# Performance work log

Measured on AMD Instinct MI355X. Metric: run time of the kernel, lower is better.

## Reference

```python
import jax, jax.numpy as jnp
import numpy as np
from jax.scipy.special import logsumexp

B, T, S, V = 64, 1024, 512, 1024


def setup_inputs() -> dict:
    key = jax.random.key(0)
    k_obs, k_emis, k_trans, k_prior = jax.random.split(key, 4)
    observations = jax.random.randint(k_obs, (B, T), 0, V, dtype=jnp.int32)
    emission_table = jax.random.normal(k_emis, (V, S), dtype=jnp.float32)
    transitions = jax.random.normal(k_trans, (S, S), dtype=jnp.float32)
    prior = jax.random.normal(k_prior, (S,), dtype=jnp.float32)
    return {
        "observations": observations,
        "emission_table": emission_table,
        "transitions": transitions,
        "prior": prior,
    }


def reference(observations, emission_table, transitions, prior):
    # alpha_0[b, s] = emission_logits(obs_0)[b, s] + prior[s]
    alpha0 = emission_table[observations[:, 0]] + prior  # [B, S]

    def step(alpha, obs_t):
        # new_alpha[b, j] = emis[b, j] + logsumexp_i(alpha[b, i] + trans[i, j])
        e = emission_table[obs_t]  # [B, S]
        a = e + logsumexp(alpha[:, :, None] + transitions[None, :, :], axis=1)
        return a, None

    # scan over time steps 1..T-1; xs is [T-1, B]
    alpha, _ = jax.lax.scan(step, alpha0, observations[:, 1:].T)
    return logsumexp(alpha, axis=1)  # [B]
```

## Files before the change

kernel.cpp:

```cpp
#include <hip/hip_runtime.h>


constexpr int Bn = 64, Tn = 1024, Sn = 512;
#define L2E 1.44269504f

typedef int v4i __attribute__((ext_vector_type(4)));

#if __has_builtin(__builtin_amdgcn_update_dpp)
template <int CTRL>
__device__ __forceinline__ float dpp_fmax(float x) {
    int s = __builtin_bit_cast(int, x);
    int d = __builtin_amdgcn_update_dpp(s, s, CTRL, 0xf, 0xf, false);
    return fmaxf(x, __builtin_bit_cast(float, d));
}
__device__ __forceinline__ float wave_max64_l63(float x) {
    x = dpp_fmax<0x121>(x);
    x = dpp_fmax<0x122>(x);
    x = dpp_fmax<0x124>(x);
    x = dpp_fmax<0x128>(x);
    x = dpp_fmax<0x142>(x);
    x = dpp_fmax<0x143>(x);
    return x;
}
__device__ __forceinline__ float wave_max64(float x) {
    return __builtin_bit_cast(float,
        __builtin_amdgcn_readlane(
            __builtin_bit_cast(int, wave_max64_l63(x)), 63));
}
#else
__device__ __forceinline__ float wave_max64(float x) {
    #pragma unroll
    for (int off = 32; off; off >>= 1) x = fmaxf(x, __shfl_xor(x, off, 64));
    return x;
}
__device__ __forceinline__ float wave_max64_l63(float x) { return wave_max64(x); }
#endif

__device__ __forceinline__ int bfrag_addr(int i, int c) {
    return ((((c >> 4) * 8 + (i >> 6)) * 64) + ((i >> 4) & 3) * 16 + (c & 15)) * 16
           + (i & 15);
}

__global__ __launch_bounds__(256) void prep_rows(
    const float* __restrict__ trans, unsigned char* __restrict__ EqB,
    float* __restrict__ rowmax)
{
    const int i = blockIdx.x;
    const int j = threadIdx.x;
    const int lane = j & 63, wv = j >> 6;
    float t0 = trans[i * Sn + j];
    float t1 = trans[i * Sn + j + 256];
    float m = fmaxf(t0, t1);
    #pragma unroll
    for (int off = 32; off; off >>= 1) m = fmaxf(m, __shfl_xor(m, off, 64));
    __shared__ float rm[4];
    if (lane == 0) rm[wv] = m;
    __syncthreads();
    m = fmaxf(fmaxf(rm[0], rm[1]), fmaxf(rm[2], rm[3]));
    if (j == 0) rowmax[i] = m;
    int q0 = __float2int_rn(127.f * __expf(t0 - m));
    int q1 = __float2int_rn(127.f * __expf(t1 - m));
    EqB[bfrag_addr(i, j)] = (unsigned char)q0;
    EqB[bfrag_addr(i, j + 256)] = (unsigned char)q1;
}

__global__ __launch_bounds__(512, 2) void hmm_fwd(
    const int* __restrict__ obs,
    const float* __restrict__ emis,
    const float* __restrict__ prior,
    const v4i* __restrict__ EqB4,
    const float* __restrict__ rowmax,
    float* __restrict__ out)
{
    const int b = blockIdx.x;
    const int tid = threadIdx.x;
    const int lane = tid & 63, wv = tid >> 6;
    const int q = lane >> 4;

    __shared__ int obs_s[Tn + 1];
    __shared__ __align__(16) unsigned char Pq[Sn];
    __shared__ __align__(16) float redm[8];
    __shared__ float reds[8];

    int o0 = obs[b * Tn + tid];
    int o1 = obs[b * Tn + 512 + tid];
    obs_s[tid] = o0;
    obs_s[tid + 512] = o1;
    if (tid == 511) obs_s[Tn] = o1;

    v4i Bf[4][8];
    #pragma unroll
    for (int tau = 0; tau < 4; ++tau)
        #pragma unroll
        for (int kap = 0; kap < 8; ++kap)
            Bf[tau][kap] = EqB4[((wv * 4 + tau) * 8 + kap) * 64 + lane];

    float rmj = rowmax[tid];
    {
        float r = wave_max64(rmj);
        if (lane == 0) redm[wv] = r;
    }
    __syncthreads();
    float RM;
    {
        float4 r0 = *(const float4*)&redm[0];
        float4 r1 = *(const float4*)&redm[4];
        RM = fmaxf(fmaxf(fmaxf(r0.x, r0.y), fmaxf(r0.z, r0.w)),
                   fmaxf(fmaxf(r1.x, r1.y), fmaxf(r1.z, r1.w)));
    }
    const float lrf = exp2f((rmj - RM) * L2E + 6.98868469f);
    const float C = RM - 9.68837417f;

    float wd = __expf(emis[obs_s[0] * Sn + tid] + prior[tid]);
    float lw = lrf * wd;
    float S = 0.f;
    float eC = emis[obs_s[1] * Sn + tid];

    for (int t = 1; t < Tn; ++t) {
        float mx = wave_max64_l63(wd);
        if (lane == 63) redm[wv] = mx;
        int oN = obs_s[t + 1];
        __syncthreads();
        float4 r0 = *(const float4*)&redm[0];
        float4 r1 = *(const float4*)&redm[4];
        float W = fmaxf(fmaxf(fmaxf(r0.x, r0.y), fmaxf(r0.z, r0.w)),
                        fmaxf(fmaxf(r1.x, r1.y), fmaxf(r1.z, r1.w)));

        float weC = __expf(eC);

        float rw = __builtin_amdgcn_rcpf(W);
        int gi = __float2int_rn(lw * rw);
        Pq[tid] = (unsigned char)gi;
        __syncthreads();

        eC = emis[oN * Sn + tid];
        S += __logf(W) + C;

        const unsigned char* Pbase = Pq + q * 16;
        v4i Af[8];
        #pragma unroll
        for (int kap = 0; kap < 8; ++kap)
            Af[kap] = *(const v4i*)(Pbase + kap * 64);

        v4i acc[4];
        #pragma unroll
        for (int tau = 0; tau < 4; ++tau) {
            v4i z = {0, 0, 0, 0};
            #pragma unroll
            for (int kap = 0; kap < 8; ++kap)
                z = __builtin_amdgcn_mfma_i32_16x16x64_i8(Af[kap], Bf[tau][kap],
                                                          z, 0, 0, 0);
            acc[tau] = z;
        }

        int idot = (lane < 16) ? acc[0].x
                 : (lane < 32) ? acc[1].x
                 : (lane < 48) ? acc[2].x
                               : acc[3].x;

        wd = weC * (float)idot;
        lw = lrf * wd;
    }

    float mw = wave_max64(wd);
    if (lane == 0) redm[wv] = mw;
    __syncthreads();
    float Wf = mw;
    #pragma unroll
    for (int w = 0; w < 8; ++w) Wf = fmaxf(Wf, redm[w]);

    float s = wd * __builtin_amdgcn_rcpf(Wf);
    #pragma unroll
    for (int off = 32; off; off >>= 1) s += __shfl_xor(s, off, 64);
    if (lane == 0) reds[wv] = s;
    __syncthreads();
    if (tid == 0) {
        float tot = 0.f;
        #pragma unroll
        for (int w = 0; w < 8; ++w) tot += reds[w];
        out[b] = S + __logf(Wf) + __logf(tot);
    }
}

extern "C" void kernel_launch(void* const* d_in, const int* in_sizes, int n_in,
                              void* d_out, int out_size, void* d_ws, size_t ws_size,
                              hipStream_t stream) {
    const int*   obs   = (const int*)d_in[0];
    const float* emis  = (const float*)d_in[1];
    const float* trans = (const float*)d_in[2];
    const float* prior = (const float*)d_in[3];
    float* out = (float*)d_out;

    unsigned char* EqB = (unsigned char*)d_ws;
    float* rowmax = (float*)(EqB + Sn * Sn);

    prep_rows<<<Sn, 256, 0, stream>>>(trans, EqB, rowmax);
    hmm_fwd<<<Bn, Sn, 0, stream>>>(obs, emis, prior,
                                   (const v4i*)EqB, rowmax, out);
}
```

Baseline: 901.7 us.

## Split int8 matvec by input slice per wave, one barrier per step

Each wave now quantizes its own 64-entry slice of alpha against a wave-local max. It packs the bytes into MFMA A-fragments in registers with DPP and ds_swizzle, and multiplies against all 512 output columns of its slice of the transition matrix. Partial integer sums go to a double-buffered LDS array and are combined per output with per-wave scale factors, which removes one of the two barriers per time step and the byte-array LDS round trip. In exchange each wave issues more MFMAs per step (32 instead of effectively 32 with dependent chains, now independent), writes more partials to LDS and adds an 8-way reduction; the per-wave quantization scale also changes numeric error.

Result: slower. 1.219 ms (+35.2%).

```diff
diff --git a/kernel.cpp b/kernel.cpp
--- a/kernel.cpp
+++ b/kernel.cpp
@@ -13,19 +13,19 @@
     int d = __builtin_amdgcn_update_dpp(s, s, CTRL, 0xf, 0xf, false);
     return fmaxf(x, __builtin_bit_cast(float, d));
 }
-__device__ __forceinline__ float wave_max64_l63(float x) {
+__device__ __forceinline__ float wave_max64(float x) {
     x = dpp_fmax<0x121>(x);
     x = dpp_fmax<0x122>(x);
     x = dpp_fmax<0x124>(x);
     x = dpp_fmax<0x128>(x);
     x = dpp_fmax<0x142>(x);
     x = dpp_fmax<0x143>(x);
-    return x;
-}
-__device__ __forceinline__ float wave_max64(float x) {
     return __builtin_bit_cast(float,
-        __builtin_amdgcn_readlane(
-            __builtin_bit_cast(int, wave_max64_l63(x)), 63));
+        __builtin_amdgcn_readlane(__builtin_bit_cast(int, x), 63));
+}
+template <int CTRL>
+__device__ __forceinline__ int dpp_mov_i(int x) {
+    return __builtin_amdgcn_update_dpp(x, x, CTRL, 0xf, 0xf, false);
 }
 #else
 __device__ __forceinline__ float wave_max64(float x) {
@@ -33,7 +33,6 @@
     for (int off = 32; off; off >>= 1) x = fmaxf(x, __shfl_xor(x, off, 64));
     return x;
 }
-__device__ __forceinline__ float wave_max64_l63(float x) { return wave_max64(x); }
 #endif
 
 __device__ __forceinline__ int bfrag_addr(int i, int c) {
@@ -75,11 +74,10 @@
     const int b = blockIdx.x;
     const int tid = threadIdx.x;
     const int lane = tid & 63, wv = tid >> 6;
-    const int q = lane >> 4;
 
     __shared__ int obs_s[Tn + 1];
-    __shared__ __align__(16) unsigned char Pq[Sn];
-    __shared__ __align__(16) float redm[8];
+    __shared__ int part[2][8][Sn];
+    __shared__ __align__(16) float redm[2][8];
     __shared__ float reds[8];
 
     int o0 = obs[b * Tn + tid];
@@ -88,23 +86,21 @@
     obs_s[tid + 512] = o1;
     if (tid == 511) obs_s[Tn] = o1;
 
-    v4i Bf[4][8];
-    #pragma unroll
-    for (int tau = 0; tau < 4; ++tau)
-        #pragma unroll
-        for (int kap = 0; kap < 8; ++kap)
-            Bf[tau][kap] = EqB4[((wv * 4 + tau) * 8 + kap) * 64 + lane];
+    v4i Bg[32];
+    #pragma unroll
+    for (int tau = 0; tau < 32; ++tau)
+        Bg[tau] = EqB4[(tau * 8 + wv) * 64 + lane];
 
     float rmj = rowmax[tid];
     {
         float r = wave_max64(rmj);
-        if (lane == 0) redm[wv] = r;
+        if (lane == 0) redm[0][wv] = r;
     }
     __syncthreads();
     float RM;
     {
-        float4 r0 = *(const float4*)&redm[0];
-        float4 r1 = *(const float4*)&redm[4];
+        float4 r0 = *(const float4*)&redm[0][0];
+        float4 r1 = *(const float4*)&redm[0][4];
         RM = fmaxf(fmaxf(fmaxf(r0.x, r0.y), fmaxf(r0.z, r0.w)),
                    fmaxf(fmaxf(r1.x, r1.y), fmaxf(r1.z, r1.w)));
     }
@@ -116,58 +112,83 @@
     float S = 0.f;
     float eC = emis[obs_s[1] * Sn + tid];
 
+    const v4i zz = {0, 0, 0, 0};
+
     for (int t = 1; t < Tn; ++t) {
-        float mx = wave_max64_l63(wd);
-        if (lane == 63) redm[wv] = mx;
+        const int pb = t & 1;
+
+        float mw = wave_max64(wd);
+        if (lane == 0) redm[pb][wv] = mw;
+        int gi = __float2int_rn(lw * __builtin_amdgcn_rcpf(mw));
+
+#if __has_builtin(__builtin_amdgcn_update_dpp)
+        int sw1 = dpp_mov_i<0xB1>(gi);
+        int sh1 = (lane & 1) << 3;
+        int P2 = (gi << sh1) | (sw1 << (8 - sh1));
+        int sw2 = dpp_mov_i<0x4E>(P2);
+        int sh2 = (lane & 2) << 3;
+        int D = (P2 << sh2) | (sw2 << (16 - sh2));
+        v4i Af;
+        Af.x = __builtin_amdgcn_ds_swizzle(D, 0x0010);
+        Af.y = __builtin_amdgcn_ds_swizzle(D, 0x0090);
+        Af.z = __builtin_amdgcn_ds_swizzle(D, 0x0110);
+        Af.w = __builtin_amdgcn_ds_swizzle(D, 0x0190);
+#else
+        v4i Af = zz;
+#endif
+
+        #pragma unroll
+        for (int bt = 0; bt < 4; ++bt) {
+            v4i acc[8];
+            #pragma unroll
+            for (int s2 = 0; s2 < 8; ++s2)
+                acc[s2] = __builtin_amdgcn_mfma_i32_16x16x64_i8(
+                              Af, Bg[bt * 8 + s2], zz, 0, 0, 0);
+            if (lane < 16) {
+                #pragma unroll
+                for (int s2 = 0; s2 < 8; ++s2)
+                    part[pb][wv][(bt * 8 + s2) * 16 + lane] = acc[s2].x;
+            }
+        }
+
         int oN = obs_s[t + 1];
         __syncthreads();
-        float4 r0 = *(const float4*)&redm[0];
-        float4 r1 = *(const float4*)&redm[4];
+
+        float4 r0 = *(const float4*)&redm[pb][0];
+        float4 r1 = *(const float4*)&redm[pb][4];
         float W = fmaxf(fmaxf(fmaxf(r0.x, r0.y), fmaxf(r0.z, r0.w)),
                         fmaxf(fmaxf(r1.x, r1.y), fmaxf(r1.z, r1.w)));
+        float rcpW = __builtin_amdgcn_rcpf(W);
+
+        int p0 = part[pb][0][tid], p1 = part[pb][1][tid];
+        int p2 = part[pb][2][tid], p3 = part[pb][3][tid];
+        int p4 = part[pb][4][tid], p5 = part[pb][5][tid];
+        int p6 = part[pb][6][tid], p7 = part[pb][7][tid];
+
+        float w0 = r0.x * rcpW, w1 = r0.y * rcpW;
+        float w2 = r0.z * rcpW, w3 = r0.w * rcpW;
+        float w4 = r1.x * rcpW, w5 = r1.y * rcpW;
+        float w6 = r1.z * rcpW, w7 = r1.w * rcpW;
+
+        float F = ((w0 * (float)p0 + w1 * (float)p1)
+                 + (w2 * (float)p2 + w3 * (float)p3))
+                + ((w4 * (float)p4 + w5 * (float)p5)
+                 + (w6 * (float)p6 + w7 * (float)p7));
 
         float weC = __expf(eC);
-
-        float rw = __builtin_amdgcn_rcpf(W);
-        int gi = __float2int_rn(lw * rw);
-        Pq[tid] = (unsigned char)gi;
-        __syncthreads();
-
+        wd = weC * F;
+        lw = lrf * wd;
+
+        S += __logf(W) + C;
         eC = emis[oN * Sn + tid];
-        S += __logf(W) + C;
-
-        const unsigned char* Pbase = Pq + q * 16;
-        v4i Af[8];
-        #pragma unroll
-        for (int kap = 0; kap < 8; ++kap)
-            Af[kap] = *(const v4i*)(Pbase + kap * 64);
-
-        v4i acc[4];
-        #pragma unroll
-        for (int tau = 0; tau < 4; ++tau) {
-            v4i z = {0, 0, 0, 0};
-            #pragma unroll
-            for (int kap = 0; kap < 8; ++kap)
-                z = __builtin_amdgcn_mfma_i32_16x16x64_i8(Af[kap], Bf[tau][kap],
-                                                          z, 0, 0, 0);
-            acc[tau] = z;
-        }
-
-        int idot = (lane < 16) ? acc[0].x
-                 : (lane < 32) ? acc[1].x
-                 : (lane < 48) ? acc[2].x
-                               : acc[3].x;
-
-        wd = weC * (float)idot;
-        lw = lrf * wd;
-    }
-
-    float mw = wave_max64(wd);
-    if (lane == 0) redm[wv] = mw;
-    __syncthreads();
-    float Wf = mw;
-    #pragma unroll
-    for (int w = 0; w < 8; ++w) Wf = fmaxf(Wf, redm[w]);
+    }
+
+    float mwf = wave_max64(wd);
+    if (lane == 0) redm[0][wv] = mwf;
+    __syncthreads();
+    float Wf = mwf;
+    #pragma unroll
+    for (int w = 0; w < 8; ++w) Wf = fmaxf(Wf, redm[0][w]);
 
     float s = wd * __builtin_amdgcn_rcpf(Wf);
     #pragma unroll
```

## Compute own-wave K-slice MFMA from registers before barrier via DPP/swizzle

Applied to the files above, without the earlier changes.

Each wave packs its own quantized probabilities into an MFMA A-fragment in registers using DPP moves and ds_swizzle. It then issues the four MFMAs for its own 64-row K-slice before the barrier, using a preloaded B fragment. The remaining seven K-slices are read from shared memory after the barrier and accumulated in interleaved order, so part of the matrix work overlaps barrier latency. The cost is extra register pressure from the BfO copy, a data-dependent skip (kap != wv) inside the unrolled loop, and added cross-lane shuffles, whose byte layout must match the fragment layout exactly.

New measurement: 1.062 ms. 17.7% more time.

```diff
diff --git a/kernel.cpp b/kernel.cpp
--- a/kernel.cpp
+++ b/kernel.cpp
@@ -26,6 +26,10 @@
     return __builtin_bit_cast(float,
         __builtin_amdgcn_readlane(
             __builtin_bit_cast(int, wave_max64_l63(x)), 63));
+}
+template <int CTRL>
+__device__ __forceinline__ int dpp_mov_i(int x) {
+    return __builtin_amdgcn_update_dpp(x, x, CTRL, 0xf, 0xf, false);
 }
 #else
 __device__ __forceinline__ float wave_max64(float x) {
@@ -95,6 +99,11 @@
         for (int kap = 0; kap < 8; ++kap)
             Bf[tau][kap] = EqB4[((wv * 4 + tau) * 8 + kap) * 64 + lane];
 
+    v4i BfO[4];
+    #pragma unroll
+    for (int tau = 0; tau < 4; ++tau)
+        BfO[tau] = EqB4[((wv * 4 + tau) * 8 + wv) * 64 + lane];
+
     float rmj = rowmax[tid];
     {
         float r = wave_max64(rmj);
@@ -115,6 +124,8 @@
     float lw = lrf * wd;
     float S = 0.f;
     float eC = emis[obs_s[1] * Sn + tid];
+
+    const v4i zz = {0, 0, 0, 0};
 
     for (int t = 1; t < Tn; ++t) {
         float mx = wave_max64_l63(wd);
@@ -131,32 +142,66 @@
         float rw = __builtin_amdgcn_rcpf(W);
         int gi = __float2int_rn(lw * rw);
         Pq[tid] = (unsigned char)gi;
+
+#if __has_builtin(__builtin_amdgcn_update_dpp)
+        int sw1 = dpp_mov_i<0xB1>(gi);
+        int sh1 = (lane & 1) << 3;
+        int P2 = (gi << sh1) | (sw1 << (8 - sh1));
+        int sw2 = dpp_mov_i<0x4E>(P2);
+        int sh2 = (lane & 2) << 3;
+        int D = (P2 << sh2) | (sw2 << (16 - sh2));
+        v4i AfO;
+        AfO.x = __builtin_amdgcn_ds_swizzle(D, 0x0010);
+        AfO.y = __builtin_amdgcn_ds_swizzle(D, 0x0090);
+        AfO.z = __builtin_amdgcn_ds_swizzle(D, 0x0110);
+        AfO.w = __builtin_amdgcn_ds_swizzle(D, 0x0190);
+
+        v4i a0 = __builtin_amdgcn_mfma_i32_16x16x64_i8(AfO, BfO[0], zz, 0, 0, 0);
+        v4i a1 = __builtin_amdgcn_mfma_i32_16x16x64_i8(AfO, BfO[1], zz, 0, 0, 0);
+        v4i a2 = __builtin_amdgcn_mfma_i32_16x16x64_i8(AfO, BfO[2], zz, 0, 0, 0);
+        v4i a3 = __builtin_amdgcn_mfma_i32_16x16x64_i8(AfO, BfO[3], zz, 0, 0, 0);
         __syncthreads();
 
         eC = emis[oN * Sn + tid];
-        S += __logf(W) + C;
 
         const unsigned char* Pbase = Pq + q * 16;
         v4i Af[8];
         #pragma unroll
         for (int kap = 0; kap < 8; ++kap)
             Af[kap] = *(const v4i*)(Pbase + kap * 64);
-
-        v4i acc[4];
-        #pragma unroll
-        for (int tau = 0; tau < 4; ++tau) {
-            v4i z = {0, 0, 0, 0};
-            #pragma unroll
-            for (int kap = 0; kap < 8; ++kap)
-                z = __builtin_amdgcn_mfma_i32_16x16x64_i8(Af[kap], Bf[tau][kap],
-                                                          z, 0, 0, 0);
-            acc[tau] = z;
+        #pragma unroll
+        for (int kap = 0; kap < 8; ++kap) {
+            if (kap != wv) {
+                a0 = __builtin_amdgcn_mfma_i32_16x16x64_i8(Af[kap], Bf[0][kap], a0, 0, 0, 0);
+                a1 = __builtin_amdgcn_mfma_i32_16x16x64_i8(Af[kap], Bf[1][kap], a1, 0, 0, 0);
+                a2 = __builtin_amdgcn_mfma_i32_16x16x64_i8(Af[kap], Bf[2][kap], a2, 0, 0, 0);
+                a3 = __builtin_amdgcn_mfma_i32_16x16x64_i8(Af[kap], Bf[3][kap], a3, 0, 0, 0);
+            }
         }
-
-        int idot = (lane < 16) ? acc[0].x
-                 : (lane < 32) ? acc[1].x
-                 : (lane < 48) ? acc[2].x
-                               : acc[3].x;
+#else
+        __syncthreads();
+        eC = emis[oN * Sn + tid];
+        const unsigned char* Pbase = Pq + q * 16;
+        v4i Af[8];
+        #pragma unroll
+        for (int kap = 0; kap < 8; ++kap)
+            Af[kap] = *(const v4i*)(Pbase + kap * 64);
+        v4i a0 = zz, a1 = zz, a2 = zz, a3 = zz;
+        #pragma unroll
+        for (int kap = 0; kap < 8; ++kap) {
+            a0 = __builtin_amdgcn_mfma_i32_16x16x64_i8(Af[kap], Bf[0][kap], a0, 0, 0, 0);
+            a1 = __builtin_amdgcn_mfma_i32_16x16x64_i8(Af[kap], Bf[1][kap], a1, 0, 0, 0);
+            a2 = __builtin_amdgcn_mfma_i32_16x16x64_i8(Af[kap], Bf[2][kap], a2, 0, 0, 0);
+            a3 = __builtin_amdgcn_mfma_i32_16x16x64_i8(Af[kap], Bf[3][kap], a3, 0, 0, 0);
+        }
+#endif
+
+        S += __logf(W) + C;
+
+        int idot = (lane < 16) ? a0.x
+                 : (lane < 32) ? a1.x
+                 : (lane < 48) ? a2.x
+                               : a3.x;
 
         wd = weC * (float)idot;
         lw = lrf * wd;
```
